# Kernel optimization log

Hardware: AMD Instinct MI355X
Metric: run time of the kernel (lower is better)

Reference implementation:

```python
import jax
import jax.numpy as jnp
import numpy as np
from jax.scipy.linalg import expm

H = 2048   # hidden_size
R = 1      # low-rank dimension
B = 2048   # batch of independent (h, x) pairs


def _glorot(key, shape):
    return jax.random.uniform(key, shape, minval=-1.0, maxval=1.0) * jnp.sqrt(2.0 / sum(shape))


def setup_inputs() -> dict:
    key = jax.random.key(0)
    k1, k2, k3, k4, k5, k6 = jax.random.split(key, 6)
    return {
        "h": jax.random.normal(k5, (B, H), dtype=jnp.float32),
        "x": jax.random.normal(k6, (B, H), dtype=jnp.float32),
        # a_diag ~ U(-1, 0) * init_scale (10.0): negative real diagonal
        "a_diag": jax.random.uniform(k1, (H,), minval=-1.0, maxval=0.0) * 10.0,
        "p_vec": _glorot(k2, (H, R)),
        "q_vec": _glorot(k3, (H, R)),
        "b_mat": _glorot(k4, (H, H)),
        "delta": jnp.array(0.1, dtype=jnp.float32),
    }


def reference(h, x, a_diag, p_vec, q_vec, b_mat, delta):
    # A = diag(a_diag) + P Q^T  (DPLR structure, materialized dense as in source)
    A = jnp.diag(a_diag) + p_vec @ q_vec.T                       # [H, H]
    # Discretized state matrix: exp(delta * A)
    expA = expm(delta * A)                                       # [H, H]
    # Discretized input matrix: A^{-1} (exp(delta A) - I) B  (pinv as in source)
    A_inv = jnp.linalg.pinv(A)                                   # [H, H]
    B_disc = A_inv @ (expA - jnp.eye(H, dtype=A.dtype)) @ b_mat  # [H, H]
    # Batched recurrence step: A h + B x  for each row of h, x
    return h @ expA.T + x @ B_disc.T                             # [B, H]
```

## Files before the change

### kernel.cpp

```cpp
#include <hip/hip_runtime.h>

#define MAXM 16
#define NL_CAP 256
#define THETA 0.04f
#define SMEM_BYTES 32768

typedef unsigned short u16;
typedef u16 u16x8 __attribute__((ext_vector_type(8)));
typedef u16 u16x4 __attribute__((ext_vector_type(4)));
typedef __bf16 bf16x8 __attribute__((ext_vector_type(8)));
typedef float f32x4 __attribute__((ext_vector_type(4)));


__device__ __forceinline__ u16 f2bf(float f) {
    unsigned u = __float_as_uint(f);
    return (u16)((u + 0x7fffu + ((u >> 16) & 1u)) >> 16);
}

__global__ __launch_bounds__(256)
void conv_k(const float* __restrict__ x, const float* __restrict__ b,
            u16* __restrict__ xb, u16* __restrict__ bb, long nx, long nb)
{
    long i = ((long)blockIdx.x * 256 + threadIdx.x) * 4;
    if (i < nx) {
        float4 v = *(const float4*)&x[i];
        u16x4 o = {f2bf(v.x), f2bf(v.y), f2bf(v.z), f2bf(v.w)};
        *(u16x4*)&xb[i] = o;
    }
    if (i < nb) {
        float4 v = *(const float4*)&b[i];
        u16x4 o = {f2bf(v.x), f2bf(v.y), f2bf(v.z), f2bf(v.w)};
        *(u16x4*)&bb[i] = o;
    }
}


__device__ __forceinline__ double frcp(double den) {
    double r = (double)__builtin_amdgcn_rcpf((float)den);
    return fma(r, fma(-den, r, 1.0), r);
}


__device__ __forceinline__ void gload_lds16(const void* g, void* l) {
    __builtin_amdgcn_global_load_lds(
        (const __attribute__((address_space(1))) unsigned int*)g,
        (__attribute__((address_space(3))) unsigned int*)l, 16, 0, 0);
}

__device__ __forceinline__ void gemm_tile(u16* Al, u16* Bl, int tid, int bx, int by,
                                          const u16* __restrict__ A,
                                          const u16* __restrict__ B,
                                          float* __restrict__ C,
                                          int Ndim, int Kstride, int Klen)
{
    const int bm = by * 128, bn = bx * 128;
    const int wv = tid >> 6, ln = tid & 63;
    const int wr = (wv >> 1) * 64, wc = (wv & 1) * 64;
    const int fr = ln & 15, fk = (ln >> 4) * 8;

    const int r0 = tid >> 2, c0 = (tid & 3) * 8;
    const u16* Ap0 = A + (size_t)(bm + r0) * Kstride + c0;
    const u16* Ap1 = Ap0 + (size_t)64 * Kstride;
    const u16* Bp0 = B + (size_t)(bn + r0) * Kstride + c0;
    const u16* Bp1 = Bp0 + (size_t)64 * Kstride;

    f32x4 acc[4][4];
#pragma unroll
    for (int m = 0; m < 4; ++m)
#pragma unroll
        for (int n = 0; n < 4; ++n) acc[m][n] = (f32x4)0.f;

    {
        u16* a0 = Al + wv * 512;
        u16* a1 = Al + 2048 + wv * 512;
        u16* b0 = Bl + wv * 512;
        u16* b1 = Bl + 2048 + wv * 512;
        gload_lds16(Ap0, a0);
        gload_lds16(Ap1, a1);
        gload_lds16(Bp0, b0);
        gload_lds16(Bp1, b1);
    }

    int cur = 0;
    for (int kk = 0; kk < Klen; kk += 32) {
        const bool hasNext = (kk + 32 < Klen);
        if (hasNext) {
            const int nb = (cur ^ 1) * 4096;
            u16* a0 = Al + nb + wv * 512;
            u16* a1 = Al + nb + 2048 + wv * 512;
            u16* b0 = Bl + nb + wv * 512;
            u16* b1 = Bl + nb + 2048 + wv * 512;
            gload_lds16(Ap0 + kk + 32, a0);
            gload_lds16(Ap1 + kk + 32, a1);
            gload_lds16(Bp0 + kk + 32, b0);
            gload_lds16(Bp1 + kk + 32, b1);
            asm volatile("s_waitcnt vmcnt(4)" ::: "memory");
        } else {
            asm volatile("s_waitcnt vmcnt(0)" ::: "memory");
        }
        __builtin_amdgcn_sched_barrier(0);
        __builtin_amdgcn_s_barrier();

        const int cb = cur * 4096;
        u16x8 af[4], bf[4];
#pragma unroll
        for (int m = 0; m < 4; ++m)
            af[m] = *(const u16x8*)&Al[cb + (wr + m * 16 + fr) * 32 + fk];
#pragma unroll
        for (int n = 0; n < 4; ++n)
            bf[n] = *(const u16x8*)&Bl[cb + (wc + n * 16 + fr) * 32 + fk];
#pragma unroll
        for (int m = 0; m < 4; ++m)
#pragma unroll
            for (int n = 0; n < 4; ++n)
                acc[m][n] = __builtin_amdgcn_mfma_f32_16x16x32_bf16(
                    __builtin_bit_cast(bf16x8, af[m]),
                    __builtin_bit_cast(bf16x8, bf[n]), acc[m][n], 0, 0, 0);

        __builtin_amdgcn_sched_barrier(0);
        __builtin_amdgcn_s_barrier();
        cur ^= 1;
    }

    const int crow = (ln >> 4) * 4;
#pragma unroll
    for (int m = 0; m < 4; ++m)
#pragma unroll
        for (int n = 0; n < 4; ++n) {
            const size_t base = (size_t)(bm + wr + m * 16 + crow) * Ndim
                              + bn + wc + n * 16 + fr;
#pragma unroll
            for (int j = 0; j < 4; ++j)
                C[base + (size_t)j * Ndim] = acc[m][n][j];
        }
}

__global__ __launch_bounds__(256)
void bgemm_k(const u16* __restrict__ A, const u16* __restrict__ B,
             float* __restrict__ C, int Ndim, int Kdim)
{
    __shared__ __align__(16) unsigned char smem[SMEM_BYTES];
    gemm_tile((u16*)smem, (u16*)smem + 8192, threadIdx.x,
              blockIdx.x, blockIdx.y, A, B, C, Ndim, Kdim, Kdim);
}


__global__ __launch_bounds__(256)
void g_sgemm_k(const float* __restrict__ A, const float* __restrict__ B,
               float* __restrict__ C, int Mdim, int Ndim, int Kdim)
{
    __shared__ __align__(16) float As[16][132];
    __shared__ __align__(16) float Bs[16][68];
    const int tid = threadIdx.x;
    const int tx = tid & 15, ty = tid >> 4;
    const int bn = blockIdx.x * 64, bm = blockIdx.y * 128;
    const int lrA = tid >> 1, lcA = (tid & 1) << 3;
    const int lrB = tid >> 2, lcB = (tid & 3) << 2;
    const float* Aptr = A + (size_t)(bm + lrA) * Kdim + lcA;
    const float* Bptr = B + (size_t)(bn + lrB) * Kdim + lcB;
    float4 a0 = *(const float4*)(Aptr);
    float4 a1 = *(const float4*)(Aptr + 4);
    float4 b0 = *(const float4*)(Bptr);
    float acc[8][4];
#pragma unroll
    for (int i = 0; i < 8; ++i)
#pragma unroll
        for (int j = 0; j < 4; ++j) acc[i][j] = 0.f;
    for (int kk = 0; kk < Kdim; kk += 16) {
        __syncthreads();
        As[lcA + 0][lrA] = a0.x; As[lcA + 1][lrA] = a0.y;
        As[lcA + 2][lrA] = a0.z; As[lcA + 3][lrA] = a0.w;
        As[lcA + 4][lrA] = a1.x; As[lcA + 5][lrA] = a1.y;
        As[lcA + 6][lrA] = a1.z; As[lcA + 7][lrA] = a1.w;
        Bs[lcB + 0][lrB] = b0.x; Bs[lcB + 1][lrB] = b0.y;
        Bs[lcB + 2][lrB] = b0.z; Bs[lcB + 3][lrB] = b0.w;
        __syncthreads();
        if (kk + 16 < Kdim) {
            a0 = *(const float4*)(Aptr + kk + 16);
            a1 = *(const float4*)(Aptr + kk + 20);
            b0 = *(const float4*)(Bptr + kk + 16);
        }
#pragma unroll
        for (int k = 0; k < 16; ++k) {
            const float4 av0 = *(const float4*)&As[k][ty * 8];
            const float4 av1 = *(const float4*)&As[k][ty * 8 + 4];
            const float4 bv  = *(const float4*)&Bs[k][tx * 4];
            const float avf[8] = {av0.x, av0.y, av0.z, av0.w, av1.x, av1.y, av1.z, av1.w};
            const float bvf[4] = {bv.x, bv.y, bv.z, bv.w};
#pragma unroll
            for (int i = 0; i < 8; ++i)
#pragma unroll
                for (int j = 0; j < 4; ++j) acc[i][j] += avf[i] * bvf[j];
        }
    }
#pragma unroll
    for (int i = 0; i < 8; ++i) {
        const int r = bm + ty * 8 + i;
        float4 v = {acc[i][0], acc[i][1], acc[i][2], acc[i][3]};
        *(float4*)&C[(size_t)r * Ndim + bn + tx * 4] = v;
    }
}


__device__ __forceinline__ double wsum(double x) {
#pragma unroll
    for (int m = 32; m; m >>= 1) x += __shfl_xor(x, m, 64);
    return x;
}
__device__ __forceinline__ float wsumf(float x) {
#pragma unroll
    for (int m = 32; m; m >>= 1) x += __shfl_xor(x, m, 64);
    return x;
}

__device__ __forceinline__ int inert(double s11, double s12, double s22,
                                     double dc, double cS)
{
    double b00 = cS - s11, b01 = -1.0 - s12, b11 = -s22;
    double det = b00 * b11 - b01 * b01, tr = b00 + b11;
    int neg = (det > 0.0) ? ((tr < 0.0) ? 2 : 0) : 1;
    return (int)(dc + 0.5) + neg - 1;
}

__device__ __forceinline__ int lane_evalN32(float tf, double td, int n4,
    const float4* l0, const float4* l1, const float4* l2,
    const double* pc, bool poly, double cS,
    double& g11o, double& g12o, double& g22o)
{
    float s11 = 0.f, s12 = 0.f, s22 = 0.f, dc = 0.f;
#pragma unroll 2
    for (int i = 0; i < n4; ++i) {
        const float4 d4 = l0[i], x4 = l1[i], y4 = l2[i];
        const float dd[4] = {d4.x, d4.y, d4.z, d4.w};
        const float xx[4] = {x4.x, x4.y, x4.z, x4.w};
        const float yy[4] = {y4.x, y4.y, y4.z, y4.w};
#pragma unroll
        for (int e = 0; e < 4; ++e) {
            float den = dd[e] - tf;
            float mag = fmaxf(fabsf(den), 1e-30f);
            den = (den < 0.f) ? -mag : mag;
            const float inv = __builtin_amdgcn_rcpf(den);
            s11 = fmaf(xx[e] * xx[e], inv, s11);
            s12 = fmaf(xx[e] * yy[e], inv, s12);
            s22 = fmaf(yy[e] * yy[e], inv, s22);
            if (dd[e] < tf) dc += 1.f;
        }
    }
    double S11 = (double)s11, S12 = (double)s12, S22 = (double)s22;
    if (poly) {
        S11 += pc[0] + td * (pc[3] + td * (pc[6] + td * pc[9]));
        S12 += pc[1] + td * (pc[4] + td * (pc[7] + td * pc[10]));
        S22 += pc[2] + td * (pc[5] + td * (pc[8] + td * pc[11]));
    }
    g11o = S11; g12o = S12; g22o = S22;
    return inert(S11, S12, S22, (double)dc, cS);
}

__device__ void spec256(unsigned char* smem, int tid,
                        const float* __restrict__ av, const float* __restrict__ pv,
                        const float* __restrict__ qv, double* __restrict__ hdr,
                        float* __restrict__ V)
{
    __builtin_amdgcn_s_setprio(1);

    float* sd2 = (float*)smem;
    float* sw1 = sd2 + 2048;
    float* sw2 = sw1 + 2048;
    float* nl0 = sw2 + 2048;
    float* nl1 = nl0 + NL_CAP;
    float* nl2 = nl1 + NL_CAP;
    double* dsh = (double*)(nl2 + NL_CAP);
    int* ish = (int*)(dsh + 192);

    const int lane = tid & 63, wv = tid >> 6;
    const int j0 = tid * 8;

    float d2r[8], w1r[8], w2r[8];
    double cS = 0, n1 = 0, n2 = 0, mx = 0;
#pragma unroll
    for (int h = 0; h < 2; ++h) {
        float4 aa = *(const float4*)&av[j0 + h * 4];
        float4 pp = *(const float4*)&pv[j0 + h * 4];
        float4 qq = *(const float4*)&qv[j0 + h * 4];
        const float a4[4] = {aa.x, aa.y, aa.z, aa.w};
        const float p4[4] = {pp.x, pp.y, pp.z, pp.w};
        const float q4[4] = {qq.x, qq.y, qq.z, qq.w};
#pragma unroll
        for (int e = 0; e < 4; ++e) {
            const int ix = h * 4 + e;
            d2r[ix] = a4[e] * a4[e];
            w1r[ix] = a4[e] * p4[e];
            w2r[ix] = q4[e];
            sd2[j0 + ix] = d2r[ix]; sw1[j0 + ix] = w1r[ix]; sw2[j0 + ix] = w2r[ix];
            cS += (double)p4[e] * p4[e];
            n1 += (double)w1r[ix] * w1r[ix];
            n2 += (double)w2r[ix] * w2r[ix];
            mx = fmax(mx, (double)d2r[ix]);
        }
    }
    cS = wsum(cS); n1 = wsum(n1); n2 = wsum(n2);
#pragma unroll
    for (int m_ = 32; m_; m_ >>= 1) mx = fmax(mx, __shfl_xor(mx, m_, 64));
    __syncthreads();
    if (lane == 0) { dsh[wv] = cS; dsh[4 + wv] = n1; dsh[8 + wv] = n2; dsh[12 + wv] = mx; }
    __syncthreads();
    cS = 0; n1 = 0; n2 = 0; mx = 0;
    for (int w = 0; w < 4; ++w) {
        cS += dsh[w]; n1 += dsh[4 + w]; n2 += dsh[8 + w];
        mx = fmax(mx, dsh[12 + w]);
    }
    __syncthreads();

    double lo = 0.0;
    double hi = mx + 0.5 * (cS + sqrt(cS * cS + 4.0)) * (n1 + n2) + 1.0;
    for (int r = 0; r < 5; ++r) {
        const double td = lo + (hi - lo) * (double)(wv + 1) / 5.0;
        const float tf = (float)td;
        float s11 = 0.f, s12 = 0.f, s22 = 0.f, dc = 0.f;
        for (int i4 = lane; i4 < 512; i4 += 64) {
            const float4 dd = ((const float4*)sd2)[i4];
            const float4 e1 = ((const float4*)sw1)[i4];
            const float4 e2 = ((const float4*)sw2)[i4];
            const float df[4] = {dd.x, dd.y, dd.z, dd.w};
            const float f1[4] = {e1.x, e1.y, e1.z, e1.w};
            const float f2[4] = {e2.x, e2.y, e2.z, e2.w};
#pragma unroll
            for (int e = 0; e < 4; ++e) {
                float den = df[e] - tf;
                float mag = fmaxf(fabsf(den), 1e-30f);
                den = (den < 0.f) ? -mag : mag;
                const float inv = __builtin_amdgcn_rcpf(den);
                s11 = fmaf(f1[e] * f1[e], inv, s11);
                s12 = fmaf(f1[e] * f2[e], inv, s12);
                s22 = fmaf(f2[e] * f2[e], inv, s22);
                if (df[e] < tf) dc += 1.f;
            }
        }
        s11 = wsumf(s11); s12 = wsumf(s12); s22 = wsumf(s22); dc = wsumf(dc);
        if (lane == 0)
            ish[wv] = inert((double)s11, (double)s12, (double)s22, (double)dc, cS);
        __syncthreads();
        double nlo = lo, nhi = hi;
        for (int i = 0; i < 4; ++i) {
            double ti = lo + (hi - lo) * (double)(i + 1) / 5.0;
            if (ish[i] >= 2048) { if (ti < nhi) nhi = ti; }
            else                { if (ti > nlo) nlo = ti; }
        }
        lo = nlo; hi = nhi;
        __syncthreads();
    }
    const double lmax = 0.5 * (lo + hi);
    const double rc = 10.0 * 2048.0 * 1.1920928955078125e-07;
    const double cut2 = rc * rc * lmax;

    int flags = 0, lc = 0;
#pragma unroll
    for (int e = 0; e < 8; ++e)
        if (d2r[e] < THETA) { flags |= (1 << e); ++lc; }
    int sc = lc;
#pragma unroll
    for (int off = 1; off < 64; off <<= 1) {
        int y = __shfl_up(sc, off, 64);
        if (lane >= off) sc += y;
    }
    const int wtot = __shfl(sc, 63, 64);
    const int excl = sc - lc;
    if (lane == 0) ish[4 + wv] = wtot;
    __syncthreads();
    int base = excl;
    for (int w = 0; w < wv; ++w) base += ish[4 + w];
    int cnt = 0;
    for (int w = 0; w < 4; ++w) cnt += ish[4 + w];
    {
        int pos = base;
#pragma unroll
        for (int e = 0; e < 8; ++e) {
            if (flags & (1 << e)) {
                if (pos < NL_CAP) { nl0[pos] = d2r[e]; nl1[pos] = w1r[e]; nl2[pos] = w2r[e]; }
                ++pos;
            }
        }
    }
    const int cntPad = (cnt + 7) & ~7;
    if (tid == 0) {
        for (int i = cnt; i < cntPad && i < NL_CAP; ++i) {
            nl0[i] = 1e30f; nl1[i] = 0.f; nl2[i] = 0.f;
        }
        ish[8] = cnt; ish[10] = cntPad >> 2;
    }

    float cff[12];
#pragma unroll
    for (int c = 0; c < 12; ++c) cff[c] = 0.f;
#pragma unroll
    for (int e = 0; e < 8; ++e) {
        if (d2r[e] >= THETA) {
            float id = __builtin_amdgcn_rcpf(d2r[e]);
            float b1 = w1r[e], b2 = w2r[e];
            float x11 = b1 * b1, x12 = b1 * b2, x22 = b2 * b2;
            float f = id;
            cff[0] += x11 * f; cff[1]  += x12 * f; cff[2]  += x22 * f; f *= id;
            cff[3] += x11 * f; cff[4]  += x12 * f; cff[5]  += x22 * f; f *= id;
            cff[6] += x11 * f; cff[7]  += x12 * f; cff[8]  += x22 * f; f *= id;
            cff[9] += x11 * f; cff[10] += x12 * f; cff[11] += x22 * f;
        }
    }
#pragma unroll
    for (int c = 0; c < 12; ++c) cff[c] = wsumf(cff[c]);
    if (lane == 0) {
        double* dw = &dsh[16 + wv * 12];
#pragma unroll
        for (int c = 0; c < 12; ++c) dw[c] = (double)cff[c];
    }
    __syncthreads();
    if (tid < 12) {
        double s = 0;
        for (int w = 0; w < 4; ++w) s += dsh[16 + w * 12 + tid];
        dsh[96 + tid] = s;
    }
    __syncthreads();

    cnt = ish[8];
    const bool nearOK = (cnt <= NL_CAP - 8);
    const float4* l0 = nearOK ? (const float4*)nl0 : (const float4*)sd2;
    const float4* l1 = nearOK ? (const float4*)nl1 : (const float4*)sw1;
    const float4* l2 = nearOK ? (const float4*)nl2 : (const float4*)sw2;
    const int n4 = nearOK ? ish[10] : 512;
    const bool poly = nearOK;
    const double* pcoef = &dsh[96];

    double zg1, zg2, zg3;
    if (wv == 0) {
        int N = lane_evalN32((float)cut2, cut2, n4, l0, l1, l2, pcoef, poly, cS,
                             zg1, zg2, zg3);
        if (lane == 0) ish[9] = N;
    }
    __syncthreads();
    int m = ish[9];
    if (m < 0) m = 0;
    if (m > MAXM) m = MAXM;

    for (int k = wv; k < m; k += 4) {
        double klo = 0.0, khi = cut2;
        for (int r = 0; r < 3; ++r) {
            const double w = khi - klo;
            const double td = klo + w * (double)(lane + 1) / 65.0;
            int N = lane_evalN32((float)td, td, n4, l0, l1, l2, pcoef, poly, cS,
                                 zg1, zg2, zg3);
            unsigned long long mask = __ballot(N >= k + 1);
            int j = (mask == 0ull) ? 64 : (__ffsll(mask) - 1);
            double nk = (j == 64) ? khi : (klo + w * (double)(j + 1) / 65.0);
            klo = klo + w * (double)j / 65.0;
            khi = nk;
        }
        const double lam = 0.5 * (klo + khi);
        double g11, g12, g22;
        lane_evalN32((float)lam, lam, n4, l0, l1, l2, pcoef, poly, cS, g11, g12, g22);
        const double m00 = 1.0 + g12, m01 = g11 + cS * g12;
        const double m10 = g22,       m11 = 1.0 + g12 + cS * g22;
        double y1, y2;
        if (m00 * m00 + m01 * m01 >= m10 * m10 + m11 * m11) { y1 = m01; y2 = -m00; }
        else                                                { y1 = m11; y2 = -m10; }
        if (lane == 0) {
            dsh[112 + 3 * k]     = lam;
            dsh[112 + 3 * k + 1] = y2;
            dsh[112 + 3 * k + 2] = y1 + cS * y2;
        }
    }
    __syncthreads();

    for (int k = 0; k < m; ++k) {
        const double lam = dsh[112 + 3 * k];
        const double z1 = dsh[112 + 3 * k + 1], z2 = dsh[112 + 3 * k + 2];
        double vr[8], pn = 0;
#pragma unroll
        for (int e = 0; e < 8; ++e) {
            double den = (double)d2r[e] - lam;
            if (fabs(den) < 1e-25) den = (den < 0 ? -1e-25 : 1e-25);
            vr[e] = ((double)w1r[e] * z1 + (double)w2r[e] * z2) * frcp(den);
            pn += vr[e] * vr[e];
        }
        pn = wsum(pn);
        if (lane == 0) dsh[160 + wv] = pn;
        __syncthreads();
        double tot = 0;
        for (int w = 0; w < 4; ++w) tot += dsh[160 + w];
        const double inv = 1.0 / sqrt(tot);
        float o0[8];
#pragma unroll
        for (int e = 0; e < 8; ++e) o0[e] = (float)(vr[e] * inv);
        *(float4*)&V[(size_t)k * 2048 + j0]     = *(float4*)&o0[0];
        *(float4*)&V[(size_t)k * 2048 + j0 + 4] = *(float4*)&o0[4];
        __syncthreads();
    }

    if (tid == 0) { hdr[0] = lmax; hdr[1] = cut2; hdr[2] = (double)m; hdr[3] = cS; }
    __builtin_amdgcn_s_setprio(0);
}


__global__ __launch_bounds__(256)
void fat_k(const u16* __restrict__ A, const u16* __restrict__ B,
           float* __restrict__ C0, float* __restrict__ C1,
           int Ndim, int Kdim, int ntiles, int nbx, int nsplit,
           const float* __restrict__ av, const float* __restrict__ pv,
           const float* __restrict__ qv, double* __restrict__ hdr,
           float* __restrict__ V)
{
    __shared__ __align__(16) unsigned char smem[SMEM_BYTES];
    const int bid = blockIdx.x;
    if (bid == 0) {
        spec256(smem, threadIdx.x, av, pv, qv, hdr, V);
        return;
    }
    if ((bid & 255) == 0) return;
    const int t = bid - 1 - (bid >> 8);
    if (t >= ntiles * nsplit) return;
    const int ks = t / ntiles;
    const int tt = t - ks * ntiles;
    const int Klen = Kdim / nsplit;
    gemm_tile((u16*)smem, (u16*)smem + 8192, threadIdx.x,
              tt % nbx, tt / nbx,
              A + (size_t)ks * Klen, B + (size_t)ks * Klen,
              ks ? C1 : C0, Ndim, Kdim, Klen);
}


__global__ __launch_bounds__(256, 2)
void series_k(float* __restrict__ io, const float* __restrict__ io2, int addP,
              const float* __restrict__ hm,
              const float* __restrict__ qv, const float* __restrict__ pv,
              const float* __restrict__ av, const float* __restrict__ delta,
              const float* __restrict__ V, const double* __restrict__ hdr,
              int useTrunc)
{
    const int lane = threadIdx.x & 63;
    const int row = blockIdx.x * 4 + (threadIdx.x >> 6);
    const float d = delta[0];
    const int m = useTrunc ? (int)hdr[2] : 0;

    float q[32], p[32], a[32], t[32], o[32];
    float* iorow = io + (size_t)row * 2048;
    const float* io2row = io2 + (size_t)row * 2048;
#pragma unroll
    for (int cc = 0; cc < 8; ++cc) {
        const int j = cc * 256 + lane * 4;
        *(float4*)&q[cc * 4] = *(const float4*)&qv[j];
        *(float4*)&p[cc * 4] = *(const float4*)&pv[j];
        *(float4*)&a[cc * 4] = *(const float4*)&av[j];
        float4 u0 = *(const float4*)&iorow[j];
        if (addP) {
            const float4 u1 = *(const float4*)&io2row[j];
            u0.x += u1.x; u0.y += u1.y; u0.z += u1.z; u0.w += u1.w;
        }
        *(float4*)&t[cc * 4] = u0;
    }
#pragma unroll
    for (int e = 0; e < 32; ++e) o[e] = t[e];

    float cf = 1.f;
    for (int k = 1; k <= 13; ++k) {
        float s = 0.f;
#pragma unroll
        for (int e = 0; e < 32; ++e) s += t[e] * q[e];
#pragma unroll
        for (int msk = 32; msk; msk >>= 1) s += __shfl_xor(s, msk, 64);
        cf /= (float)(k + 1);
        const float ds = d * s;
#pragma unroll
        for (int e = 0; e < 32; ++e) { t[e] = d * a[e] * t[e] + ds * p[e]; o[e] += cf * t[e]; }
    }
#pragma unroll
    for (int e = 0; e < 32; ++e) o[e] *= d;

    for (int k = 0; k < m; ++k) {
        const float* vr = V + (size_t)k * 2048;
        float vk[32];
#pragma unroll
        for (int cc = 0; cc < 8; ++cc)
            *(float4*)&vk[cc * 4] = *(const float4*)&vr[cc * 256 + lane * 4];
        float s = 0.f;
#pragma unroll
        for (int e = 0; e < 32; ++e) s += o[e] * vk[e];
#pragma unroll
        for (int msk = 32; msk; msk >>= 1) s += __shfl_xor(s, msk, 64);
#pragma unroll
        for (int e = 0; e < 32; ++e) o[e] -= s * vk[e];
    }

    const float* hrow = hm + (size_t)row * 2048;
#pragma unroll
    for (int cc = 0; cc < 8; ++cc)
        *(float4*)&t[cc * 4] = *(const float4*)&hrow[cc * 256 + lane * 4];
#pragma unroll
    for (int e = 0; e < 32; ++e) o[e] += t[e];
    cf = 1.f;
    for (int k = 1; k <= 14; ++k) {
        float s = 0.f;
#pragma unroll
        for (int e = 0; e < 32; ++e) s += t[e] * q[e];
#pragma unroll
        for (int msk = 32; msk; msk >>= 1) s += __shfl_xor(s, msk, 64);
        cf /= (float)k;
        const float ds = d * s;
#pragma unroll
        for (int e = 0; e < 32; ++e) { t[e] = d * a[e] * t[e] + ds * p[e]; o[e] += cf * t[e]; }
    }
#pragma unroll
    for (int cc = 0; cc < 8; ++cc)
        *(float4*)&iorow[cc * 256 + lane * 4] = *(const float4*)&o[cc * 4];
}


extern "C" void kernel_launch(void* const* d_in, const int* in_sizes, int n_in,
                              void* d_out, int out_size, void* d_ws, size_t ws_size,
                              hipStream_t stream)
{
    const float* hmat  = (const float*)d_in[0];
    const float* xmat  = (const float*)d_in[1];
    const float* adiag = (const float*)d_in[2];
    const float* pvec  = (const float*)d_in[3];
    const float* qvec  = (const float*)d_in[4];
    const float* bmat  = (const float*)d_in[5];
    const float* delta = (const float*)d_in[6];
    float* out = (float*)d_out;

    const int H  = in_sizes[2];
    const int Bb = in_sizes[0] / H;
    const size_t SZ = (size_t)Bb * H;
    const size_t HH = (size_t)H * H;

    double* hdr = (double*)d_ws;
    float* V = (float*)(hdr + 8);
    u16* xb = (u16*)(V + (size_t)MAXM * H);
    u16* bb = xb + SZ;
    float* C1 = (float*)(bb + HH);

    const size_t needSpec  = 64 + (size_t)MAXM * H * sizeof(float);
    const size_t needFull  = needSpec + (SZ + HH) * sizeof(u16);
    const size_t needSplit = needFull + SZ * sizeof(float);
    const bool doTrunc = (H == 2048) && (ws_size >= needSpec);
    const bool doBf16  = (ws_size >= needFull) && (H % 128 == 0) && (Bb % 128 == 0);
    const bool doSplit = doBf16 && doTrunc && (ws_size >= needSplit) && (H % 64 == 0);

    dim3 blk256(256);
    const int nbx = H / 128;
    const int ntiles = nbx * (Bb / 128);

    if (doBf16) {
        const long nmax = (long)(SZ > HH ? SZ : HH);
        const int cg = (int)((nmax / 4 + 255) / 256);
        conv_k<<<cg, blk256, 0, stream>>>(xmat, bmat, xb, bb, (long)SZ, (long)HH);
        if (doTrunc) {
            const int nsplit = doSplit ? 2 : 1;
            const int NT = ntiles * nsplit;
            const int grid = 1 + NT + (NT + 254) / 255;
            fat_k<<<grid, blk256, 0, stream>>>(
                xb, bb, out, C1, H, H, ntiles, nbx, nsplit,
                adiag, pvec, qvec, hdr, V);
        } else {
            dim3 gg(nbx, Bb / 128);
            bgemm_k<<<gg, blk256, 0, stream>>>(xb, bb, out, H, H);
        }
    } else {
        if (doTrunc)
            fat_k<<<1, blk256, 0, stream>>>(nullptr, nullptr, out, nullptr,
                                            H, H, 0, 1, 1,
                                            adiag, pvec, qvec, hdr, V);
        dim3 gg(H / 64, Bb / 128);
        g_sgemm_k<<<gg, blk256, 0, stream>>>(xmat, bmat, out, Bb, H, H);
    }

    series_k<<<Bb / 4, blk256, 0, stream>>>(out, doSplit ? C1 : out,
                                            doSplit ? 1 : 0,
                                            hmat, qvec, pvec, adiag, delta,
                                            V, hdr, doTrunc ? 1 : 0);
}
```

Measured before the change: 79.44 us.

## Cut bisection rounds, lower THETA, and move eigenvector build to fp32

Lowers the THETA threshold, raises the unroll factor of the secular-function evaluation loop, and drops one of three bisection refinement rounds used to locate eigenvalues. The eigenvector construction now normalizes z, then computes components, norms and reciprocals in fp32 with hardware rcp instead of fp64. These changes target fp64 throughput and the serial cost of the eigen-solver phase. In exchange, eigenvalue localization is coarser and eigenvectors lose precision, which may hurt accuracy.

```diff
diff --git a/kernel.cpp b/kernel.cpp
--- a/kernel.cpp
+++ b/kernel.cpp
@@ -2,7 +2,7 @@
 
 #define MAXM 16
 #define NL_CAP 256
-#define THETA 0.04f
+#define THETA 0.02f
 #define SMEM_BYTES 32768
 
 typedef unsigned short u16;
@@ -228,7 +228,7 @@
     double& g11o, double& g12o, double& g22o)
 {
     float s11 = 0.f, s12 = 0.f, s22 = 0.f, dc = 0.f;
-#pragma unroll 2
+#pragma unroll 4
     for (int i = 0; i < n4; ++i) {
         const float4 d4 = l0[i], x4 = l1[i], y4 = l2[i];
         const float dd[4] = {d4.x, d4.y, d4.z, d4.w};
@@ -442,7 +442,7 @@
 
     for (int k = wv; k < m; k += 4) {
         double klo = 0.0, khi = cut2;
-        for (int r = 0; r < 3; ++r) {
+        for (int r = 0; r < 2; ++r) {
             const double w = khi - klo;
             const double td = klo + w * (double)(lane + 1) / 65.0;
             int N = lane_evalN32((float)td, td, n4, l0, l1, l2, pcoef, poly, cS,
@@ -461,34 +461,41 @@
         double y1, y2;
         if (m00 * m00 + m01 * m01 >= m10 * m10 + m11 * m11) { y1 = m01; y2 = -m00; }
         else                                                { y1 = m11; y2 = -m10; }
+        double z1 = y2, z2 = y1 + cS * y2;
+        const double zs = 1.0 / fmax(fmax(fabs(z1), fabs(z2)), 1e-300);
         if (lane == 0) {
             dsh[112 + 3 * k]     = lam;
-            dsh[112 + 3 * k + 1] = y2;
-            dsh[112 + 3 * k + 2] = y1 + cS * y2;
+            dsh[112 + 3 * k + 1] = z1 * zs;
+            dsh[112 + 3 * k + 2] = z2 * zs;
         }
     }
     __syncthreads();
 
     for (int k = 0; k < m; ++k) {
         const double lam = dsh[112 + 3 * k];
-        const double z1 = dsh[112 + 3 * k + 1], z2 = dsh[112 + 3 * k + 2];
-        double vr[8], pn = 0;
+        const float z1 = (float)dsh[112 + 3 * k + 1];
+        const float z2 = (float)dsh[112 + 3 * k + 2];
+        float vr[8];
+        float pn = 0.f;
 #pragma unroll
         for (int e = 0; e < 8; ++e) {
-            double den = (double)d2r[e] - lam;
-            if (fabs(den) < 1e-25) den = (den < 0 ? -1e-25 : 1e-25);
-            vr[e] = ((double)w1r[e] * z1 + (double)w2r[e] * z2) * frcp(den);
-            pn += vr[e] * vr[e];
-        }
-        pn = wsum(pn);
-        if (lane == 0) dsh[160 + wv] = pn;
+            const double dend = (double)d2r[e] - lam;
+            float den = (float)dend;
+            float mag = fmaxf(fabsf(den), 1e-12f);
+            den = (den < 0.f) ? -mag : mag;
+            const float vi = (w1r[e] * z1 + w2r[e] * z2) * __builtin_amdgcn_rcpf(den);
+            pn = fmaf(vi, vi, pn);
+            vr[e] = vi;
+        }
+        pn = wsumf(pn);
+        if (lane == 0) dsh[160 + wv] = (double)pn;
         __syncthreads();
         double tot = 0;
         for (int w = 0; w < 4; ++w) tot += dsh[160 + w];
-        const double inv = 1.0 / sqrt(tot);
+        const float inv = (float)(1.0 / sqrt(tot));
         float o0[8];
 #pragma unroll
-        for (int e = 0; e < 8; ++e) o0[e] = (float)(vr[e] * inv);
+        for (int e = 0; e < 8; ++e) o0[e] = vr[e] * inv;
         *(float4*)&V[(size_t)k * 2048 + j0]     = *(float4*)&o0[0];
         *(float4*)&V[(size_t)k * 2048 + j0 + 4] = *(float4*)&o0[4];
         __syncthreads();
```

New measurement: 77.39 us. 1.03x faster.
